# Kernel optimization log

Measured on AMD Instinct MI355X. Metric: run time of the kernel, lower is better.

## Reference

```python
import jax, jax.numpy as jnp
import numpy as np

DIM = 512
HEADS = 8
HEAD_DIM = DIM // HEADS
MLP_HIDDEN = int(DIM * 4.0)
B, N = 4, 2048
LS_INIT = 1e-5
EPS = 1e-5


def _layernorm(x, w, b):
    mu = jnp.mean(x, axis=-1, keepdims=True)
    var = jnp.mean(jnp.square(x - mu), axis=-1, keepdims=True)
    return (x - mu) * jax.lax.rsqrt(var + EPS) * w + b


def setup_inputs() -> dict:
    key = jax.random.key(0)
    ks = jax.random.split(key, 12)
    s = 0.02
    return {
        "x": jax.random.normal(ks[0], (B, N, DIM), jnp.float32),
        "rel_pos_bias": jax.random.normal(ks[1], (HEADS, N, N), jnp.float32),
        "qkv_w": jax.random.normal(ks[2], (DIM, 3 * DIM), jnp.float32) * s,
        "qkv_b": jnp.zeros((3 * DIM,), jnp.float32),
        "out_w": jax.random.normal(ks[3], (DIM, DIM), jnp.float32) * s,
        "out_b": jnp.zeros((DIM,), jnp.float32),
        "ln1_w": jnp.ones((DIM,), jnp.float32),
        "ln1_b": jnp.zeros((DIM,), jnp.float32),
        "ln2_w": jnp.ones((DIM,), jnp.float32),
        "ln2_b": jnp.zeros((DIM,), jnp.float32),
        "ffn_w1": jax.random.normal(ks[4], (DIM, MLP_HIDDEN), jnp.float32) * s,
        "ffn_b1": jnp.zeros((MLP_HIDDEN,), jnp.float32),
        "ffn_w2": jax.random.normal(ks[5], (MLP_HIDDEN, DIM), jnp.float32) * s,
        "ffn_b2": jnp.zeros((DIM,), jnp.float32),
        "gamma1": jnp.full((DIM,), LS_INIT, jnp.float32),
        "gamma2": jnp.full((DIM,), LS_INIT, jnp.float32),
    }


def reference(x, rel_pos_bias, qkv_w, qkv_b, out_w, out_b, ln1_w, ln1_b,
              ln2_w, ln2_b, ffn_w1, ffn_b1, ffn_w2, ffn_b2, gamma1, gamma2):
    # Pre-norm MHA with relative-position bias
    y = _layernorm(x, ln1_w, ln1_b)                       # [B,N,C]
    qkv = y @ qkv_w + qkv_b                               # [B,N,3C]
    qkv = qkv.reshape(B, N, 3, HEADS, HEAD_DIM)
    q = jnp.transpose(qkv[:, :, 0], (0, 2, 1, 3))         # [B,H,N,D]
    k = jnp.transpose(qkv[:, :, 1], (0, 2, 1, 3))
    v = jnp.transpose(qkv[:, :, 2], (0, 2, 1, 3))
    scale = 1.0 / np.sqrt(HEAD_DIM).astype(np.float32)
    attn = jnp.einsum("bhid,bhjd->bhij", q, k) * scale    # [B,H,N,N]
    attn = attn + rel_pos_bias[None]
    attn = jax.nn.softmax(attn, axis=-1)
    out = jnp.einsum("bhij,bhjd->bhid", attn, v)          # [B,H,N,D]
    out = jnp.transpose(out, (0, 2, 1, 3)).reshape(B, N, DIM)
    out = out @ out_w + out_b
    x = x + out * gamma1                                  # layer scale, no drop-path (eval)
    # FFN with exact GELU
    y2 = _layernorm(x, ln2_w, ln2_b)
    h = jax.nn.gelu(y2 @ ffn_w1 + ffn_b1, approximate=False)
    ffn_out = h @ ffn_w2 + ffn_b2
    x = x + ffn_out * gamma2
    return x
```

## Files before the change

### kernel.cpp

```cpp
#include <hip/hip_runtime.h>
#include <hip/hip_bf16.h>
#include <math.h>

#define SEQ 2048
#define BATCH 4
#define DM 512
#define NH 8
#define HD 64
#define HID 2048
#define ROWS (BATCH * SEQ)

typedef __attribute__((ext_vector_type(8))) short short8;
typedef __attribute__((ext_vector_type(4))) float f32x4;

__device__ __forceinline__ short f2bf(float f) {
    unsigned u = __float_as_uint(f);
    u += 0x7fff + ((u >> 16) & 1);
    return (short)(u >> 16);
}

__device__ __forceinline__ void gl2lds16(const void* g, void* l) {
    __builtin_amdgcn_global_load_lds(
        (const __attribute__((address_space(1))) void*)g,
        (__attribute__((address_space(3))) void*)l, 16, 0, 0);
}

__global__ __launch_bounds__(256) void tcast_all(
    const float* __restrict__ qkv_w, const float* __restrict__ out_w,
    const float* __restrict__ w1, const float* __restrict__ w2,
    short* __restrict__ o_qkv, short* __restrict__ o_out,
    short* __restrict__ o_w1, short* __restrict__ o_w2) {
    __shared__ float tile[32][33];
    int id = blockIdx.x;
    const float* W; short* O; int K, N;
    if (id < 768)       { W = qkv_w; O = o_qkv; K = 512;  N = 1536; }
    else if (id < 1024) { W = out_w; O = o_out; K = 512;  N = 512;  id -= 768; }
    else if (id < 2048) { W = w1;    O = o_w1;  K = 512;  N = 2048; id -= 1024; }
    else                { W = w2;    O = o_w2;  K = 2048; N = 512;  id -= 2048; }
    int tn = N / 32;
    int n0 = (id % tn) * 32, k0 = (id / tn) * 32;
    int tx = threadIdx.x, ty = threadIdx.y;
#pragma unroll
    for (int i = 0; i < 4; ++i)
        tile[ty + i * 8][tx] = W[(size_t)(k0 + ty + i * 8) * N + n0 + tx];
    __syncthreads();
#pragma unroll
    for (int i = 0; i < 4; ++i)
        O[(size_t)(n0 + ty + i * 8) * K + k0 + tx] = f2bf(tile[tx][ty + i * 8]);
}

__global__ __launch_bounds__(256) void ln_k(const float* __restrict__ X,
                                            const float* __restrict__ g,
                                            const float* __restrict__ bta,
                                            short* __restrict__ Y) {
    int t = threadIdx.x;
    int wv = t >> 6, ln = t & 63;
    size_t row = (size_t)blockIdx.x * 4 + wv;
    const float* xr = X + row * DM;
    float4 v0 = *(const float4*)(xr + ln * 4);
    float4 v1 = *(const float4*)(xr + 256 + ln * 4);
    float s = v0.x + v0.y + v0.z + v0.w + v1.x + v1.y + v1.z + v1.w;
    float q = v0.x * v0.x + v0.y * v0.y + v0.z * v0.z + v0.w * v0.w +
              v1.x * v1.x + v1.y * v1.y + v1.z * v1.z + v1.w * v1.w;
#pragma unroll
    for (int off = 1; off < 64; off <<= 1) {
        s += __shfl_xor(s, off);
        q += __shfl_xor(q, off);
    }
    float mean = s * (1.0f / 512.0f);
    float var = q * (1.0f / 512.0f) - mean * mean;
    float rstd = rsqrtf(var + 1e-5f);
    int c0 = ln * 4, c1 = 256 + ln * 4;
    ushort4 o0, o1;
    o0.x = (unsigned short)f2bf((v0.x - mean) * rstd * g[c0 + 0] + bta[c0 + 0]);
    o0.y = (unsigned short)f2bf((v0.y - mean) * rstd * g[c0 + 1] + bta[c0 + 1]);
    o0.z = (unsigned short)f2bf((v0.z - mean) * rstd * g[c0 + 2] + bta[c0 + 2]);
    o0.w = (unsigned short)f2bf((v0.w - mean) * rstd * g[c0 + 3] + bta[c0 + 3]);
    o1.x = (unsigned short)f2bf((v1.x - mean) * rstd * g[c1 + 0] + bta[c1 + 0]);
    o1.y = (unsigned short)f2bf((v1.y - mean) * rstd * g[c1 + 1] + bta[c1 + 1]);
    o1.z = (unsigned short)f2bf((v1.z - mean) * rstd * g[c1 + 2] + bta[c1 + 2]);
    o1.w = (unsigned short)f2bf((v1.w - mean) * rstd * g[c1 + 3] + bta[c1 + 3]);
    *(ushort4*)((unsigned short*)Y + row * DM + c0) = o0;
    *(ushort4*)((unsigned short*)Y + row * DM + c1) = o1;
}

template <int EPI, int TN>
__global__ __launch_bounds__(256) void gemm_bt(const short* __restrict__ A,
                                               const short* __restrict__ Bt,
                                               const float* __restrict__ bias,
                                               const float* __restrict__ gamma,
                                               const float* __restrict__ res,
                                               void* __restrict__ Cout,
                                               int M, int N, int K, int gx) {
    constexpr int NI = TN / 32;
    __shared__ __attribute__((aligned(16))) short As0[128][32];
    __shared__ __attribute__((aligned(16))) short As1[128][32];
    __shared__ __attribute__((aligned(16))) short Bs0[TN][32];
    __shared__ __attribute__((aligned(16))) short Bs1[TN][32];
    int t = threadIdx.x;
    int w = t >> 6, ln = t & 63;
    int quad = ln >> 4, l15 = ln & 15;
    int nwg = gridDim.x;
    int qq = nwg >> 3;
    int sw = ((blockIdx.x & 7) * qq) + (blockIdx.x >> 3);
    int bx = sw % gx, by = sw / gx;
    int n0 = bx * TN, m0 = by * 128;
    int wm = (w & 1) * 64, wn = (w >> 1) * (TN / 2);

    int srow0 = w * 32 + (ln >> 2);
    int srow1 = srow0 + 16;
    int srowB = w * 16 + (ln >> 2);
    int schunk = (ln & 3) * 8;
    const short* Ag0 = A + (size_t)(m0 + srow0) * K + schunk;
    const short* Ag1 = A + (size_t)(m0 + srow1) * K + schunk;
    const short* Bg0 = Bt + (size_t)(n0 + srow0) * K + schunk;
    const short* Bg1 = Bt + (size_t)(n0 + srow1) * K + schunk;
    const short* BgB = Bt + (size_t)(n0 + srowB) * K + schunk;

    f32x4 acc[4][NI];
#pragma unroll
    for (int i = 0; i < 4; ++i)
#pragma unroll
        for (int j = 0; j < NI; ++j) acc[i][j] = (f32x4){0.f, 0.f, 0.f, 0.f};

    for (int k0 = 0; k0 < K; k0 += 64) {
        __syncthreads();
        gl2lds16(Ag0 + k0, &As0[srow0][schunk]);
        gl2lds16(Ag1 + k0, &As0[srow1][schunk]);
        gl2lds16(Ag0 + k0 + 32, &As1[srow0][schunk]);
        gl2lds16(Ag1 + k0 + 32, &As1[srow1][schunk]);
        if (TN == 128) {
            gl2lds16(Bg0 + k0, &Bs0[srow0 & (TN - 1)][schunk]);
            gl2lds16(Bg1 + k0, &Bs0[srow1 & (TN - 1)][schunk]);
            gl2lds16(Bg0 + k0 + 32, &Bs1[srow0 & (TN - 1)][schunk]);
            gl2lds16(Bg1 + k0 + 32, &Bs1[srow1 & (TN - 1)][schunk]);
        } else {
            gl2lds16(BgB + k0, &Bs0[srowB & (TN - 1)][schunk]);
            gl2lds16(BgB + k0 + 32, &Bs1[srowB & (TN - 1)][schunk]);
        }
        __syncthreads();
        {
            short8 af[4], bf[NI];
#pragma unroll
            for (int mi = 0; mi < 4; ++mi)
                af[mi] = *(const short8*)&As0[wm + mi * 16 + l15][quad * 8];
#pragma unroll
            for (int ni = 0; ni < NI; ++ni)
                bf[ni] = *(const short8*)&Bs0[wn + ni * 16 + l15][quad * 8];
#pragma unroll
            for (int mi = 0; mi < 4; ++mi)
#pragma unroll
                for (int ni = 0; ni < NI; ++ni)
                    acc[mi][ni] = __builtin_amdgcn_mfma_f32_16x16x32_bf16(
                        af[mi], bf[ni], acc[mi][ni], 0, 0, 0);
        }
        {
            short8 af[4], bf[NI];
#pragma unroll
            for (int mi = 0; mi < 4; ++mi)
                af[mi] = *(const short8*)&As1[wm + mi * 16 + l15][quad * 8];
#pragma unroll
            for (int ni = 0; ni < NI; ++ni)
                bf[ni] = *(const short8*)&Bs1[wn + ni * 16 + l15][quad * 8];
#pragma unroll
            for (int mi = 0; mi < 4; ++mi)
#pragma unroll
                for (int ni = 0; ni < NI; ++ni)
                    acc[mi][ni] = __builtin_amdgcn_mfma_f32_16x16x32_bf16(
                        af[mi], bf[ni], acc[mi][ni], 0, 0, 0);
        }
    }

#pragma unroll
    for (int mi = 0; mi < 4; ++mi) {
#pragma unroll
        for (int ni = 0; ni < NI; ++ni) {
#pragma unroll
            for (int r = 0; r < 4; ++r) {
                int row = m0 + wm + mi * 16 + quad * 4 + r;
                int col = n0 + wn + ni * 16 + l15;
                float v = acc[mi][ni][r] + bias[col];
                if (EPI == 0) {
                    ((short*)Cout)[(size_t)row * N + col] = f2bf(v);
                } else if (EPI == 1) {
                    float u = v * fmaf(v * v, 0.0713548162f, 1.59576912f);
                    float gg = v / (1.0f + __expf(-u));
                    ((short*)Cout)[(size_t)row * N + col] = f2bf(gg);
                } else {
                    ((float*)Cout)[(size_t)row * N + col] =
                        fmaf(v, gamma[col], res[(size_t)row * N + col]);
                }
            }
        }
    }
}

__global__ __launch_bounds__(256) void qkvbias_k(
    const short* __restrict__ A, const short* __restrict__ Bt,
    const float* __restrict__ qkvb, short* __restrict__ Cout,
    short* __restrict__ Cout2,
    const float* __restrict__ bias, short* __restrict__ biasP) {
    __shared__ __attribute__((aligned(16))) char smem[33024];
    int bid = blockIdx.x;
    int grp = bid / 11, sub = bid % 11;
    int t = threadIdx.x;
    int w = t >> 6, ln = t & 63;
    int quad = ln >> 4, l15 = ln & 15;

    if (sub < 3) {
        typedef short (*tile32)[32];
        tile32 As0 = (tile32)smem;
        tile32 As1 = (tile32)(smem + 8192);
        tile32 Bs0 = (tile32)(smem + 16384);
        tile32 Bs1 = (tile32)(smem + 24576);
        const int K = 512, N = 1536;
        int g = grp * 3 + sub;
        int n0 = (g % 12) * 128, m0 = (g / 12) * 128;
        int wm = (w & 1) * 64, wn = (w >> 1) * 64;

        int srow0 = w * 32 + (ln >> 2);
        int srow1 = srow0 + 16;
        int schunk = (ln & 3) * 8;
        const short* Ag0 = A + (size_t)(m0 + srow0) * K + schunk;
        const short* Ag1 = A + (size_t)(m0 + srow1) * K + schunk;
        const short* Bg0 = Bt + (size_t)(n0 + srow0) * K + schunk;
        const short* Bg1 = Bt + (size_t)(n0 + srow1) * K + schunk;

        f32x4 acc[4][4];
#pragma unroll
        for (int i = 0; i < 4; ++i)
#pragma unroll
            for (int j = 0; j < 4; ++j) acc[i][j] = (f32x4){0.f, 0.f, 0.f, 0.f};

        for (int k0 = 0; k0 < K; k0 += 64) {
            __syncthreads();
            gl2lds16(Ag0 + k0, &As0[srow0][schunk]);
            gl2lds16(Ag1 + k0, &As0[srow1][schunk]);
            gl2lds16(Ag0 + k0 + 32, &As1[srow0][schunk]);
            gl2lds16(Ag1 + k0 + 32, &As1[srow1][schunk]);
            gl2lds16(Bg0 + k0, &Bs0[srow0][schunk]);
            gl2lds16(Bg1 + k0, &Bs0[srow1][schunk]);
            gl2lds16(Bg0 + k0 + 32, &Bs1[srow0][schunk]);
            gl2lds16(Bg1 + k0 + 32, &Bs1[srow1][schunk]);
            __syncthreads();
            {
                short8 af[4], bf[4];
#pragma unroll
                for (int mi = 0; mi < 4; ++mi)
                    af[mi] = *(const short8*)&As0[wm + mi * 16 + l15][quad * 8];
#pragma unroll
                for (int ni = 0; ni < 4; ++ni)
                    bf[ni] = *(const short8*)&Bs0[wn + ni * 16 + l15][quad * 8];
#pragma unroll
                for (int mi = 0; mi < 4; ++mi)
#pragma unroll
                    for (int ni = 0; ni < 4; ++ni)
                        acc[mi][ni] = __builtin_amdgcn_mfma_f32_16x16x32_bf16(
                            af[mi], bf[ni], acc[mi][ni], 0, 0, 0);
            }
            {
                short8 af[4], bf[4];
#pragma unroll
                for (int mi = 0; mi < 4; ++mi)
                    af[mi] = *(const short8*)&As1[wm + mi * 16 + l15][quad * 8];
#pragma unroll
                for (int ni = 0; ni < 4; ++ni)
                    bf[ni] = *(const short8*)&Bs1[wn + ni * 16 + l15][quad * 8];
#pragma unroll
                for (int mi = 0; mi < 4; ++mi)
#pragma unroll
                    for (int ni = 0; ni < 4; ++ni)
                        acc[mi][ni] = __builtin_amdgcn_mfma_f32_16x16x32_bf16(
                            af[mi], bf[ni], acc[mi][ni], 0, 0, 0);
            }
        }

        if (n0 >= 1024) {
#pragma unroll
            for (int mi = 0; mi < 4; ++mi) {
#pragma unroll
                for (int ni = 0; ni < 4; ++ni) {
                    int col = n0 + wn + ni * 16 + l15;
                    int d = col - 1024, hh = d >> 6, dd = d & 63;
                    int row0 = m0 + wm + mi * 16 + quad * 4;
                    int bb = row0 >> 11, key = row0 & 2047;
                    float bs = qkvb[col];
                    ushort4 pk;
                    pk.x = (unsigned short)f2bf(acc[mi][ni][0] + bs);
                    pk.y = (unsigned short)f2bf(acc[mi][ni][1] + bs);
                    pk.z = (unsigned short)f2bf(acc[mi][ni][2] + bs);
                    pk.w = (unsigned short)f2bf(acc[mi][ni][3] + bs);
                    *(ushort4*)&Cout2[((size_t)(bb * 8 + hh) * 64 + dd) * 2048 + key] = pk;
                }
            }
        } else {
#pragma unroll
            for (int mi = 0; mi < 4; ++mi) {
#pragma unroll
                for (int ni = 0; ni < 4; ++ni) {
#pragma unroll
                    for (int r = 0; r < 4; ++r) {
                        int row = m0 + wm + mi * 16 + quad * 4 + r;
                        int col = n0 + wn + ni * 16 + l15;
                        float v = acc[mi][ni][r] + qkvb[col];
                        float sc = (n0 < 512) ? 0.18033688f : 1.0f;
                        Cout[(size_t)row * 1024 + col] = f2bf(v * sc);
                    }
                }
            }
        }
    } else {
        typedef short (*tile1032)[1032];
        tile1032 tl = (tile1032)smem;
        int id = grp * 8 + (sub - 3);
        int half = id & 1;
        int g = (id >> 1) & 127;
        int h = id >> 8;
        const float* src = bias + (size_t)h * SEQ * SEQ + (size_t)g * 16 * SEQ + half * 1024;
#pragma unroll
        for (int i = 0; i < 16; ++i) {
            float4 v = *(const float4*)(src + (size_t)i * SEQ + t * 4);
            float2 lo, hi;
            lo.x = v.x * 1.44269504f; lo.y = v.y * 1.44269504f;
            hi.x = v.z * 1.44269504f; hi.y = v.w * 1.44269504f;
            __hip_bfloat162 l2 = __float22bfloat162_rn(lo);
            __hip_bfloat162 h2 = __float22bfloat162_rn(hi);
            uint2 pp;
            pp.x = *(unsigned*)&l2;
            pp.y = *(unsigned*)&h2;
            *(uint2*)&tl[i][t * 4] = pp;
        }
        __syncthreads();
        int jtbase = half * 16;
#pragma unroll
        for (int u = 0; u < 4; ++u) {
            int jl = w * 4 + u;
            int tau = (h * 128 + g) * 32 + jtbase + jl;
#pragma unroll
            for (int n2 = 0; n2 < 2; ++n2) {
                uint2 a = *(const uint2*)&tl[l15][jl * 64 + n2 * 32 + quad * 4];
                uint2 b = *(const uint2*)&tl[l15][jl * 64 + n2 * 32 + 16 + quad * 4];
                uint4 pp;
                pp.x = a.x; pp.y = a.y; pp.z = b.x; pp.w = b.y;
                *(uint4*)(biasP + (size_t)tau * 1024 + n2 * 512 + ln * 8) = pp;
            }
        }
    }
}

__global__ __launch_bounds__(256, 3) void attn_k(const short* __restrict__ qkv,
                                                 const short* __restrict__ vT,
                                                 const short* __restrict__ biasP,
                                                 short* __restrict__ Aout) {
    __shared__ __attribute__((aligned(16))) short Ks[2][64 * 64];
    __shared__ __attribute__((aligned(16))) short Vs[2][64 * 64];
    __shared__ __attribute__((aligned(16))) short Ps[4][2][16 * 64];
    int t = threadIdx.x;
    int w = t >> 6, ln = t & 63, quad = ln >> 4, l15 = ln & 15;
    int idx = blockIdx.x;
    int h = idx & 7, b = (idx >> 3) & 3, qt = idx >> 5;
    int qb = qt * 128 + w * 16;
    const size_t cbase = (size_t)b * SEQ * 1024;

    const short* qrow0 = qkv + cbase + (size_t)(qb + l15) * 1024 + h * 64;
    const short* qrow1 = qrow0 + (size_t)64 * 1024;
    short8 qf[2][2];
    qf[0][0] = *(const short8*)(qrow0 + quad * 8);
    qf[0][1] = *(const short8*)(qrow0 + 32 + quad * 8);
    qf[1][0] = *(const short8*)(qrow1 + quad * 8);
    qf[1][1] = *(const short8*)(qrow1 + 32 + quad * 8);

    int kr = t >> 3, kc = t & 7;
    int sc = (kc ^ (kr & 7)) * 8;
    const short* kgS = qkv + cbase + 512 + h * 64 + sc;
    const short* vgS = vT + (size_t)(b * 8 + h) * 64 * 2048 + sc;

    int g0 = qt * 8 + w;
    const short* bp0 = biasP + ((size_t)(h * 128 + g0) * 32) * 1024 + ln * 8;
    const short* bp1 = biasP + ((size_t)(h * 128 + g0 + 4) * 32) * 1024 + ln * 8;

    short8 ones;
#pragma unroll
    for (int i = 0; i < 8; ++i) ones[i] = (short)0x3F80;

    f32x4 o[2][4], ol[2];
#pragma unroll
    for (int qg = 0; qg < 2; ++qg) {
#pragma unroll
        for (int db = 0; db < 4; ++db) o[qg][db] = (f32x4){0.f, 0.f, 0.f, 0.f};
        ol[qg] = (f32x4){0.f, 0.f, 0.f, 0.f};
    }

    int sw7 = l15 & 7;

    gl2lds16(kgS,                              &Ks[0][t * 8]);
    gl2lds16(kgS + (size_t)32 * 1024,          &Ks[0][2048 + t * 8]);
    gl2lds16(vgS,                              &Vs[0][t * 8]);
    gl2lds16(vgS + (size_t)32 * 2048,          &Vs[0][2048 + t * 8]);
    uint4 bbc[2][2];
#pragma unroll
    for (int n2 = 0; n2 < 2; ++n2) {
        bbc[0][n2] = *(const uint4*)(bp0 + n2 * 512);
        bbc[1][n2] = *(const uint4*)(bp1 + n2 * 512);
    }

    int cur = 0;
    for (int jt = 0; jt < 32; ++jt) {
        __syncthreads();
        int jn = (jt < 31) ? (jt + 1) : jt;
        int j1 = jn * 64;
        int nxt = cur ^ 1;
        gl2lds16(kgS + (size_t)(j1 + kr) * 1024,      &Ks[nxt][t * 8]);
        gl2lds16(kgS + (size_t)(j1 + 32 + kr) * 1024, &Ks[nxt][2048 + t * 8]);
        gl2lds16(vgS + (size_t)kr * 2048 + j1,        &Vs[nxt][t * 8]);
        gl2lds16(vgS + (size_t)(32 + kr) * 2048 + j1, &Vs[nxt][2048 + t * 8]);

        f32x4 s4[2][4];
#pragma unroll
        for (int ni = 0; ni < 4; ++ni) {
            short8 k0 = *(const short8*)&Ks[cur][(ni * 16 + l15) * 64 + ((quad ^ sw7) * 8)];
            short8 k1 = *(const short8*)&Ks[cur][(ni * 16 + l15) * 64 + (((4 + quad) ^ sw7) * 8)];
#pragma unroll
            for (int qg = 0; qg < 2; ++qg) {
                uint4 bb = bbc[qg][ni >> 1];
                unsigned lo = (ni & 1) ? bb.z : bb.x;
                unsigned hi = (ni & 1) ? bb.w : bb.y;
                f32x4 z;
                z[0] = __uint_as_float(lo << 16);
                z[1] = __uint_as_float(lo & 0xffff0000u);
                z[2] = __uint_as_float(hi << 16);
                z[3] = __uint_as_float(hi & 0xffff0000u);
                z = __builtin_amdgcn_mfma_f32_16x16x32_bf16(k0, qf[qg][0], z, 0, 0, 0);
                s4[qg][ni] = __builtin_amdgcn_mfma_f32_16x16x32_bf16(k1, qf[qg][1], z, 0, 0, 0);
            }
        }
#pragma unroll
        for (int n2 = 0; n2 < 2; ++n2) {
            bbc[0][n2] = *(const uint4*)(bp0 + (size_t)jn * 1024 + n2 * 512);
            bbc[1][n2] = *(const uint4*)(bp1 + (size_t)jn * 1024 + n2 * 512);
        }
#pragma unroll
        for (int qg = 0; qg < 2; ++qg) {
#pragma unroll
            for (int ni = 0; ni < 4; ++ni) {
                float2 plo, phi;
                plo.x = exp2f(s4[qg][ni][0]);
                plo.y = exp2f(s4[qg][ni][1]);
                phi.x = exp2f(s4[qg][ni][2]);
                phi.y = exp2f(s4[qg][ni][3]);
                __hip_bfloat162 l2 = __float22bfloat162_rn(plo);
                __hip_bfloat162 h2 = __float22bfloat162_rn(phi);
                union { uint2 u; } pp;
                pp.u.x = *(unsigned*)&l2;
                pp.u.y = *(unsigned*)&h2;
                int c = ni * 2 + (quad >> 1);
                *(uint2*)&Ps[w][qg][l15 * 64 + ((c ^ sw7) * 8) + (quad & 1) * 4] = pp.u;
            }
        }
#pragma unroll
        for (int kk = 0; kk < 2; ++kk) {
            short8 ap0 = *(const short8*)&Ps[w][0][l15 * 64 + (((kk * 4 + quad) ^ sw7) * 8)];
            short8 ap1 = *(const short8*)&Ps[w][1][l15 * 64 + (((kk * 4 + quad) ^ sw7) * 8)];
#pragma unroll
            for (int db = 0; db < 4; ++db) {
                short8 vv = *(const short8*)&Vs[cur][(db * 16 + l15) * 64 + (((kk * 4 + quad) ^ sw7) * 8)];
                o[0][db] = __builtin_amdgcn_mfma_f32_16x16x32_bf16(ap0, vv, o[0][db], 0, 0, 0);
                o[1][db] = __builtin_amdgcn_mfma_f32_16x16x32_bf16(ap1, vv, o[1][db], 0, 0, 0);
            }
            ol[0] = __builtin_amdgcn_mfma_f32_16x16x32_bf16(ap0, ones, ol[0], 0, 0, 0);
            ol[1] = __builtin_amdgcn_mfma_f32_16x16x32_bf16(ap1, ones, ol[1], 0, 0, 0);
        }
        cur = nxt;
    }
#pragma unroll
    for (int qg = 0; qg < 2; ++qg) {
#pragma unroll
        for (int r = 0; r < 4; ++r) {
            float inv = 1.0f / ol[qg][r];
            int qrow_g = b * SEQ + qb + qg * 64 + quad * 4 + r;
#pragma unroll
            for (int db = 0; db < 4; ++db) {
                Aout[(size_t)qrow_g * DM + h * 64 + db * 16 + l15] =
                    f2bf(o[qg][db][r] * inv);
            }
        }
    }
}

extern "C" void kernel_launch(void* const* d_in, const int* in_sizes, int n_in,
                              void* d_out, int out_size, void* d_ws, size_t ws_size,
                              hipStream_t stream) {
    const float* x      = (const float*)d_in[0];
    const float* bias   = (const float*)d_in[1];
    const float* qkv_w  = (const float*)d_in[2];
    const float* qkv_b  = (const float*)d_in[3];
    const float* out_w  = (const float*)d_in[4];
    const float* out_b  = (const float*)d_in[5];
    const float* ln1_w  = (const float*)d_in[6];
    const float* ln1_b  = (const float*)d_in[7];
    const float* ln2_w  = (const float*)d_in[8];
    const float* ln2_b  = (const float*)d_in[9];
    const float* ffn_w1 = (const float*)d_in[10];
    const float* ffn_b1 = (const float*)d_in[11];
    const float* ffn_w2 = (const float*)d_in[12];
    const float* ffn_b2 = (const float*)d_in[13];
    const float* gamma1 = (const float*)d_in[14];
    const float* gamma2 = (const float*)d_in[15];
    float* out = (float*)d_out;

    short* wqkvT = (short*)d_ws;
    short* woutT = wqkvT + (size_t)1536 * 512;
    short* w1T   = woutT + (size_t)512 * 512;
    short* w2T   = w1T + (size_t)2048 * 512;
    short* y1    = w2T + (size_t)512 * 2048;
    short* qkvB  = y1 + (size_t)ROWS * DM;
    short* vTb   = qkvB + (size_t)ROWS * 1024;
    short* aoutB = vTb + (size_t)32 * 64 * 2048;
    float* x1    = (float*)(aoutB + (size_t)ROWS * DM);
    short* biasPw = (short*)(x1 + (size_t)ROWS * DM);
    short* hB    = qkvB;

    tcast_all<<<3072, dim3(32, 8), 0, stream>>>(qkv_w, out_w, ffn_w1, ffn_w2,
                                                wqkvT, woutT, w1T, w2T);
    ln_k<<<ROWS / 4, 256, 0, stream>>>(x, ln1_w, ln1_b, y1);
    qkvbias_k<<<2816, 256, 0, stream>>>(y1, wqkvT, qkv_b, qkvB, vTb,
                                        bias, biasPw);
    attn_k<<<512, 256, 0, stream>>>(qkvB, vTb, biasPw, aoutB);
    gemm_bt<2, 128><<<256, 256, 0, stream>>>(
        aoutB, woutT, out_b, gamma1, x, x1, ROWS, 512, 512, 4);
    ln_k<<<ROWS / 4, 256, 0, stream>>>(x1, ln2_w, ln2_b, y1);
    gemm_bt<1, 128><<<1024, 256, 0, stream>>>(
        y1, w1T, ffn_b1, nullptr, nullptr, hB, ROWS, 2048, 512, 16);
    gemm_bt<2, 128><<<256, 256, 0, stream>>>(
        hB, w2T, ffn_b2, gamma2, x1, out, ROWS, 512, 2048, 4);
}
```

Baseline: 438.6 us.

## Double-buffer GEMM LDS tiles to overlap global loads with MFMA

Splits the GEMM shared-memory tiles into two ping-pong buffers. The loads for the next K-step are issued before the MFMAs on the current step, so global-to-LDS traffic overlaps compute. This leaves one barrier per iteration instead of two. It doubles LDS use per block, which may lower occupancy. Correctness depends on the barrier making the async global_load_lds writes visible; the code adds no explicit vmcnt wait.

Measured after the change: 431.4 us. About the same (-1.6%).

```diff
diff --git a/kernel.cpp b/kernel.cpp
--- a/kernel.cpp
+++ b/kernel.cpp
@@ -93,10 +93,8 @@
                                                void* __restrict__ Cout,
                                                int M, int N, int K, int gx) {
     constexpr int NI = TN / 32;
-    __shared__ __attribute__((aligned(16))) short As0[128][32];
-    __shared__ __attribute__((aligned(16))) short As1[128][32];
-    __shared__ __attribute__((aligned(16))) short Bs0[TN][32];
-    __shared__ __attribute__((aligned(16))) short Bs1[TN][32];
+    __shared__ __attribute__((aligned(16))) short As[2][2][128][32];
+    __shared__ __attribute__((aligned(16))) short Bs[2][2][TN][32];
     int t = threadIdx.x;
     int w = t >> 6, ln = t & 63;
     int quad = ln >> 4, l15 = ln & 15;
@@ -123,30 +121,38 @@
 #pragma unroll
         for (int j = 0; j < NI; ++j) acc[i][j] = (f32x4){0.f, 0.f, 0.f, 0.f};
 
-    for (int k0 = 0; k0 < K; k0 += 64) {
-        __syncthreads();
-        gl2lds16(Ag0 + k0, &As0[srow0][schunk]);
-        gl2lds16(Ag1 + k0, &As0[srow1][schunk]);
-        gl2lds16(Ag0 + k0 + 32, &As1[srow0][schunk]);
-        gl2lds16(Ag1 + k0 + 32, &As1[srow1][schunk]);
+    auto STAGE = [&](int buf, int k0) {
+        gl2lds16(Ag0 + k0, &As[buf][0][srow0][schunk]);
+        gl2lds16(Ag1 + k0, &As[buf][0][srow1][schunk]);
+        gl2lds16(Ag0 + k0 + 32, &As[buf][1][srow0][schunk]);
+        gl2lds16(Ag1 + k0 + 32, &As[buf][1][srow1][schunk]);
         if (TN == 128) {
-            gl2lds16(Bg0 + k0, &Bs0[srow0 & (TN - 1)][schunk]);
-            gl2lds16(Bg1 + k0, &Bs0[srow1 & (TN - 1)][schunk]);
-            gl2lds16(Bg0 + k0 + 32, &Bs1[srow0 & (TN - 1)][schunk]);
-            gl2lds16(Bg1 + k0 + 32, &Bs1[srow1 & (TN - 1)][schunk]);
+            gl2lds16(Bg0 + k0, &Bs[buf][0][srow0 & (TN - 1)][schunk]);
+            gl2lds16(Bg1 + k0, &Bs[buf][0][srow1 & (TN - 1)][schunk]);
+            gl2lds16(Bg0 + k0 + 32, &Bs[buf][1][srow0 & (TN - 1)][schunk]);
+            gl2lds16(Bg1 + k0 + 32, &Bs[buf][1][srow1 & (TN - 1)][schunk]);
         } else {
-            gl2lds16(BgB + k0, &Bs0[srowB & (TN - 1)][schunk]);
-            gl2lds16(BgB + k0 + 32, &Bs1[srowB & (TN - 1)][schunk]);
-        }
-        __syncthreads();
-        {
+            gl2lds16(BgB + k0, &Bs[buf][0][srowB & (TN - 1)][schunk]);
+            gl2lds16(BgB + k0 + 32, &Bs[buf][1][srowB & (TN - 1)][schunk]);
+        }
+    };
+
+    STAGE(0, 0);
+    __syncthreads();
+
+    int NS = K >> 6;
+    for (int s = 0; s < NS; ++s) {
+        int cur = s & 1;
+        if (s + 1 < NS) STAGE(cur ^ 1, (s + 1) << 6);
+#pragma unroll
+        for (int hh = 0; hh < 2; ++hh) {
             short8 af[4], bf[NI];
 #pragma unroll
             for (int mi = 0; mi < 4; ++mi)
-                af[mi] = *(const short8*)&As0[wm + mi * 16 + l15][quad * 8];
+                af[mi] = *(const short8*)&As[cur][hh][wm + mi * 16 + l15][quad * 8];
 #pragma unroll
             for (int ni = 0; ni < NI; ++ni)
-                bf[ni] = *(const short8*)&Bs0[wn + ni * 16 + l15][quad * 8];
+                bf[ni] = *(const short8*)&Bs[cur][hh][wn + ni * 16 + l15][quad * 8];
 #pragma unroll
             for (int mi = 0; mi < 4; ++mi)
 #pragma unroll
@@ -154,21 +160,7 @@
                     acc[mi][ni] = __builtin_amdgcn_mfma_f32_16x16x32_bf16(
                         af[mi], bf[ni], acc[mi][ni], 0, 0, 0);
         }
-        {
-            short8 af[4], bf[NI];
-#pragma unroll
-            for (int mi = 0; mi < 4; ++mi)
-                af[mi] = *(const short8*)&As1[wm + mi * 16 + l15][quad * 8];
-#pragma unroll
-            for (int ni = 0; ni < NI; ++ni)
-                bf[ni] = *(const short8*)&Bs1[wn + ni * 16 + l15][quad * 8];
-#pragma unroll
-            for (int mi = 0; mi < 4; ++mi)
-#pragma unroll
-                for (int ni = 0; ni < NI; ++ni)
-                    acc[mi][ni] = __builtin_amdgcn_mfma_f32_16x16x32_bf16(
-                        af[mi], bf[ni], acc[mi][ni], 0, 0, 0);
-        }
+        __syncthreads();
     }
 
 #pragma unroll
```
